# Kernel optimization log

Measured on AMD Instinct MI355X. Metric: run time of the kernel, lower is better.

The kernel has to match this reference:

```python
import jax, jax.numpy as jnp
import numpy as np

B, T, D = 2, 4096, 512
H, K = 8, 64
F = 2048
EPS = 1e-5


def _layer_norm(x, scale, offset):
    mean = jnp.mean(x, axis=-1, keepdims=True)
    var = jnp.var(x, axis=-1, keepdims=True)
    inv = scale * jax.lax.rsqrt(var + EPS)
    return (x - mean) * inv + offset


def setup_inputs() -> dict:
    key = jax.random.key(0)
    ks = jax.random.split(key, 12)
    s = lambda fan_in: (2.0 / fan_in) ** 0.5  # VarianceScaling(2.0) std
    inputs = jax.random.normal(ks[0], (B, T, D), jnp.float32)
    return {
        "inputs": inputs,
        "ln1_scale": jnp.ones((D,), jnp.float32),
        "ln1_offset": jnp.zeros((D,), jnp.float32),
        "wq": jax.random.normal(ks[1], (D, H * K), jnp.float32) * s(D),
        "bq": jnp.zeros((H * K,), jnp.float32),
        "wk": jax.random.normal(ks[2], (D, H * K), jnp.float32) * s(D),
        "bk": jnp.zeros((H * K,), jnp.float32),
        "wv": jax.random.normal(ks[3], (D, H * K), jnp.float32) * s(D),
        "bv": jnp.zeros((H * K,), jnp.float32),
        "wo": jax.random.normal(ks[4], (H * K, D), jnp.float32) * s(H * K),
        "bo": jnp.zeros((D,), jnp.float32),
        "ln2_scale": jnp.ones((D,), jnp.float32),
        "ln2_offset": jnp.zeros((D,), jnp.float32),
        "w1": jax.random.normal(ks[5], (D, F), jnp.float32) * (1.0 / D) ** 0.5,
        "b1": jnp.zeros((F,), jnp.float32),
        "w2": jax.random.normal(ks[6], (F, D), jnp.float32) * (1.0 / F) ** 0.5,
        "b2": jnp.zeros((D,), jnp.float32),
    }


def reference(inputs, ln1_scale, ln1_offset, wq, bq, wk, bk, wv, bv, wo, bo,
              ln2_scale, ln2_offset, w1, b1, w2, b2):
    # --- pre-attention LayerNorm ---
    x1 = _layer_norm(inputs, ln1_scale, ln1_offset)
    # --- multi-head attention (eval mode, no mask) ---
    q = (x1 @ wq + bq).reshape(B, T, H, K)
    k = (x1 @ wk + bk).reshape(B, T, H, K)
    v = (x1 @ wv + bv).reshape(B, T, H, K)
    logits = jnp.einsum('bthd,bshd->bhts', q, k) / jnp.sqrt(jnp.asarray(K, q.dtype))
    attn = jax.nn.softmax(logits, axis=-1)
    ctx = jnp.einsum('bhts,bshd->bthd', attn, v).reshape(B, T, H * K)
    attn_out = ctx @ wo + bo
    # --- residual ---
    x = inputs + attn_out
    # --- pre-FFN LayerNorm + GELU FFN ---
    y = _layer_norm(x, ln2_scale, ln2_offset)
    ff = jax.nn.gelu(y @ w1 + b1) @ w2 + b2
    return x + ff
```

## Files before the change

### kernel.cpp

```cpp
#include <hip/hip_runtime.h>
#include <hip/hip_bf16.h>

typedef __attribute__((ext_vector_type(4))) float f32x4;
typedef __attribute__((ext_vector_type(8))) short short8;

#define DEV __device__ __forceinline__

DEV short f2bf(float f) {
    union { float f; unsigned u; } a; a.f = f;
    unsigned r = a.u + 0x7fffu + ((a.u >> 16) & 1u);
    return (short)(r >> 16);
}

DEV float bf2f(short s) {
    union { unsigned u; float f; } a;
    a.u = ((unsigned)(unsigned short)s) << 16;
    return a.f;
}

DEV unsigned cvt_pk_bf16(float a, float b) {
    unsigned r;
    asm("v_cvt_pk_bf16_f32 %0, %1, %2" : "=v"(r) : "v"(a), "v"(b));
    return r;
}

DEV float exp2_fast(float x) { return __builtin_amdgcn_exp2f(x); }

DEV void gload16(const short* g, short* l) {
    __builtin_amdgcn_global_load_lds(
        (__attribute__((address_space(1))) void*)g,
        (__attribute__((address_space(3))) void*)l, 16, 0, 0);
}

DEV float gelu_f(float x) {
    float u = 0.7978845608028654f * (x + 0.044715f * x * x * x);
    float e = __expf(2.0f * u);
    float t = 1.0f - 2.0f / (e + 1.0f);
    return 0.5f * x * (1.0f + t);
}

__global__ __launch_bounds__(256) void ln_kernel(const float* __restrict__ x,
                                                 const float* __restrict__ scale,
                                                 const float* __restrict__ offset,
                                                 short* __restrict__ out) {
    const int wid = threadIdx.x >> 6, lane = threadIdx.x & 63;
    const long row = (long)blockIdx.x * 4 + wid;
    const float* xr = x + row * 512;
    f32x4 v0 = *(const f32x4*)&xr[lane * 8];
    f32x4 v1 = *(const f32x4*)&xr[lane * 8 + 4];
    float s = 0.f, sq = 0.f;
#pragma unroll
    for (int i = 0; i < 4; i++) {
        s += v0[i] + v1[i];
        sq += v0[i] * v0[i] + v1[i] * v1[i];
    }
#pragma unroll
    for (int m = 1; m < 64; m <<= 1) { s += __shfl_xor(s, m); sq += __shfl_xor(sq, m); }
    float mean = s * (1.0f / 512.0f);
    float var = sq * (1.0f / 512.0f) - mean * mean;
    float inv = rsqrtf(var + 1e-5f);
    f32x4 sc0 = *(const f32x4*)&scale[lane * 8];
    f32x4 sc1 = *(const f32x4*)&scale[lane * 8 + 4];
    f32x4 of0 = *(const f32x4*)&offset[lane * 8];
    f32x4 of1 = *(const f32x4*)&offset[lane * 8 + 4];
    short8 o;
#pragma unroll
    for (int i = 0; i < 4; i++) {
        o[i]     = f2bf((v0[i] - mean) * inv * sc0[i] + of0[i]);
        o[4 + i] = f2bf((v1[i] - mean) * inv * sc1[i] + of1[i]);
    }
    *(short8*)&out[row * 512 + lane * 8] = o;
}

__global__ __launch_bounds__(256) void prep_kernel(const float* __restrict__ wq,
                                                   const float* __restrict__ wk,
                                                   const float* __restrict__ wv,
                                                   const float* __restrict__ wo,
                                                   const float* __restrict__ w1,
                                                   const float* __restrict__ w2,
                                                   const float* __restrict__ bq,
                                                   const float* __restrict__ bk,
                                                   const float* __restrict__ bv,
                                                   short* __restrict__ wqkvt,
                                                   short* __restrict__ wot,
                                                   short* __restrict__ w1t,
                                                   short* __restrict__ w2t,
                                                   float* __restrict__ bqkv) {
    const int bid = blockIdx.x;
    if (bid == 768) {
        for (int i = threadIdx.x; i < 512; i += 256) {
            bqkv[i] = bq[i]; bqkv[512 + i] = bk[i]; bqkv[1024 + i] = bv[i];
        }
        return;
    }
    const float* src; short* dst; int Kd, N, kt, nt;
    if (bid < 256) {
        Kd = 512; N = 512;
        const int which = bid >> 6, local = bid & 63;
        kt = local & 7; nt = local >> 3;
        if (which == 0)      { src = wq; dst = wqkvt; }
        else if (which == 1) { src = wk; dst = wqkvt + 512 * 512; }
        else if (which == 2) { src = wv; dst = wqkvt + 2 * 512 * 512; }
        else                 { src = wo; dst = wot; }
    } else if (bid < 512) {
        src = w1; dst = w1t; Kd = 512; N = 2048;
        const int local = bid - 256; kt = local & 7; nt = local >> 3;
    } else {
        src = w2; dst = w2t; Kd = 2048; N = 512;
        const int local = bid - 512; kt = local & 31; nt = local >> 5;
    }
    __shared__ float tile[64][65];
    const int k0 = kt * 64, n0 = nt * 64;
    const int tid = threadIdx.x;
#pragma unroll
    for (int ld = 0; ld < 4; ld++) {
        int li = ld * 1024 + tid * 4;
        int r = li >> 6, c = li & 63;
        f32x4 tv = *(const f32x4*)&src[(long)(k0 + r) * N + n0 + c];
        tile[r][c] = tv[0]; tile[r][c + 1] = tv[1];
        tile[r][c + 2] = tv[2]; tile[r][c + 3] = tv[3];
    }
    __syncthreads();
#pragma unroll
    for (int st = 0; st < 2; st++) {
        int li = st * 2048 + tid * 8;
        int r = li >> 6, c = li & 63;
        short8 o;
#pragma unroll
        for (int i = 0; i < 8; i++) o[i] = f2bf(tile[c + i][r]);
        *(short8*)&dst[(long)(n0 + r) * Kd + k0 + c] = o;
    }
}

template <int BM, bool GELU_ACT, bool OUT_BF16, bool RESID>
__global__ __launch_bounds__(256) void gemm_bt(const short* __restrict__ A,
                                               const short* __restrict__ Bt,
                                               const float* __restrict__ bias,
                                               const float* __restrict__ resid,
                                               void* __restrict__ Cout,
                                               int M, int N, int Kd) {
    constexpr int NR = (BM == 128) ? 4 : 2;
    constexpr int LA = BM / 32;
    __shared__ short Asm[BM][64];
    __shared__ short Bsm[128][64];
    const int tid = threadIdx.x;
    const int wid = tid >> 6, lane = tid & 63;
    const int lr = lane & 15, lg = lane >> 4;
    const int row0 = blockIdx.x * BM, col0 = blockIdx.y * 128;
    const int wm = (BM == 128) ? (wid >> 1) * 64 : 0;
    const int wn = (BM == 128) ? (wid & 1) * 64 : wid * 32;

    f32x4 acc[4][NR];
#pragma unroll
    for (int m = 0; m < 4; m++)
#pragma unroll
        for (int n = 0; n < NR; n++)
#pragma unroll
            for (int j = 0; j < 4; j++) acc[m][n][j] = 0.f;

    const int swr = (lr & 7) << 3;

    for (int k0 = 0; k0 < Kd; k0 += 64) {
#pragma unroll
        for (int ld = 0; ld < LA; ld++) {
            int off = ld * 2048 + tid * 8;
            int r = off >> 6, c = off & 63;
            int sc = c ^ ((r & 7) << 3);
            gload16(&A[(long)(row0 + r) * Kd + k0 + sc], &Asm[0][0] + off);
        }
#pragma unroll
        for (int ld = 0; ld < 4; ld++) {
            int off = ld * 2048 + tid * 8;
            int r = off >> 6, c = off & 63;
            int sc = c ^ ((r & 7) << 3);
            gload16(&Bt[(long)(col0 + r) * Kd + k0 + sc], &Bsm[0][0] + off);
        }
        __syncthreads();
#pragma unroll
        for (int kk = 0; kk < 64; kk += 32) {
            short8 af[4], bf[NR];
#pragma unroll
            for (int m = 0; m < 4; m++) af[m] = *(const short8*)&Asm[wm + m * 16 + lr][(kk + lg * 8) ^ swr];
#pragma unroll
            for (int n = 0; n < NR; n++) bf[n] = *(const short8*)&Bsm[wn + n * 16 + lr][(kk + lg * 8) ^ swr];
#pragma unroll
            for (int m = 0; m < 4; m++)
#pragma unroll
                for (int n = 0; n < NR; n++)
                    acc[m][n] = __builtin_amdgcn_mfma_f32_16x16x32_bf16(af[m], bf[n], acc[m][n], 0, 0, 0);
        }
        __syncthreads();
    }

#pragma unroll
    for (int m = 0; m < 4; m++) {
#pragma unroll
        for (int n = 0; n < NR; n++) {
#pragma unroll
            for (int j = 0; j < 4; j++) {
                int r = row0 + wm + m * 16 + lg * 4 + j;
                int c = col0 + wn + n * 16 + lr;
                float v = acc[m][n][j] + bias[c];
                if constexpr (GELU_ACT) v = gelu_f(v);
                if constexpr (RESID) v += resid[(long)r * N + c];
                if constexpr (OUT_BF16) ((short*)Cout)[(long)r * N + c] = f2bf(v);
                else                    ((float*)Cout)[(long)r * N + c] = v;
            }
        }
    }
}

__global__ __launch_bounds__(256) void attn_kernel(const short* __restrict__ q,
                                                   const short* __restrict__ k,
                                                   const short* __restrict__ v,
                                                   float* __restrict__ opart,
                                                   float* __restrict__ mpart,
                                                   float* __restrict__ lpart) {
    __shared__ short Ksm[128][64];
    __shared__ short Vsm[64][136];
    __shared__ short Psm[4][16][136];
    const int tid = threadIdx.x, wid = tid >> 6, lane = tid & 63;
    const int lr = lane & 15, lg = lane >> 4;
    const int bh = blockIdx.y, b = bh >> 3, h = bh & 7;
    const int t0 = blockIdx.x * 128;
    const int split = blockIdx.z;
    const int s_begin = split * 2048, s_end = s_begin + 2048;
    const long base = (long)b * 4096 * 1536 + h * 64;

    short8 qf[2][2];
#pragma unroll
    for (int rg = 0; rg < 2; rg++) {
        const long qoff = base + (long)(t0 + wid * 32 + rg * 16 + lr) * 1536 + lg * 8;
        short8 q0 = *(const short8*)&q[qoff];
        short8 q1 = *(const short8*)&q[qoff + 32];
#pragma unroll
        for (int i = 0; i < 8; i++) {
            qf[rg][0][i] = f2bf(bf2f(q0[i]) * 0.18033688f);
            qf[rg][1][i] = f2bf(bf2f(q1[i]) * 0.18033688f);
        }
    }

    f32x4 o[2][4];
    float mrow[8], lrow[8];
#pragma unroll
    for (int rg = 0; rg < 2; rg++)
#pragma unroll
        for (int n = 0; n < 4; n++)
#pragma unroll
            for (int j = 0; j < 4; j++) o[rg][n][j] = 0.f;
#pragma unroll
    for (int j = 0; j < 8; j++) { mrow[j] = -1e30f; lrow[j] = 0.f; }

    const int skey = tid >> 3, sd = (tid & 7) * 8, sm = tid & 7;
    short8 kreg[4], vreg[4];
#pragma unroll
    for (int p = 0; p < 4; p++) {
        long off = base + (long)(s_begin + p * 32 + skey) * 1536 + sd;
        kreg[p] = *(const short8*)&k[off];
        vreg[p] = *(const short8*)&v[off];
    }

    for (int s0 = s_begin; s0 < s_end; s0 += 128) {
        __syncthreads();
#pragma unroll
        for (int p = 0; p < 4; p++) {
            int key = p * 32 + skey;
            *(short8*)&Ksm[key][sd ^ ((key & 7) << 3)] = kreg[p];
            int kc = key ^ (sm << 3);
#pragma unroll
            for (int i = 0; i < 8; i++) Vsm[sd + i][kc] = vreg[p][i];
        }
        __syncthreads();
        if (s0 + 128 < s_end) {
#pragma unroll
            for (int p = 0; p < 4; p++) {
                long off = base + (long)(s0 + 128 + p * 32 + skey) * 1536 + sd;
                kreg[p] = *(const short8*)&k[off];
                vreg[p] = *(const short8*)&v[off];
            }
        }

        const int ksw = (lr & 7) << 3;
#pragma unroll
        for (int rg = 0; rg < 2; rg++) {
            f32x4 s[8];
#pragma unroll
            for (int c = 0; c < 8; c++) { s[c][0] = 0.f; s[c][1] = 0.f; s[c][2] = 0.f; s[c][3] = 0.f; }
            __builtin_amdgcn_s_setprio(1);
#pragma unroll
            for (int c = 0; c < 8; c++) {
                const int krow = c * 16 + lr;
                short8 kf0 = *(const short8*)&Ksm[krow][(lg * 8) ^ ksw];
                short8 kf1 = *(const short8*)&Ksm[krow][(32 + lg * 8) ^ ksw];
                s[c] = __builtin_amdgcn_mfma_f32_16x16x32_bf16(qf[rg][0], kf0, s[c], 0, 0, 0);
                s[c] = __builtin_amdgcn_mfma_f32_16x16x32_bf16(qf[rg][1], kf1, s[c], 0, 0, 0);
            }
            __builtin_amdgcn_s_setprio(0);

#pragma unroll
            for (int j = 0; j < 4; j++) {
                const int r8 = rg * 4 + j;
                float m01 = fmaxf(s[0][j], s[1][j]), m23 = fmaxf(s[2][j], s[3][j]);
                float m45 = fmaxf(s[4][j], s[5][j]), m67 = fmaxf(s[6][j], s[7][j]);
                float mx = fmaxf(fmaxf(m01, m23), fmaxf(m45, m67));
                mx = fmaxf(mx, __shfl_xor(mx, 1));
                mx = fmaxf(mx, __shfl_xor(mx, 2));
                mx = fmaxf(mx, __shfl_xor(mx, 4));
                mx = fmaxf(mx, __shfl_xor(mx, 8));
                float mn = mrow[r8];
                if (!__all(mx <= mn + 8.0f)) {
                    mn = fmaxf(mrow[r8], mx);
                    float alpha = exp2_fast(mrow[r8] - mn);
                    mrow[r8] = mn;
                    lrow[r8] *= alpha;
#pragma unroll
                    for (int n = 0; n < 4; n++) o[rg][n][j] *= alpha;
                }
                float rs = 0.f;
#pragma unroll
                for (int c = 0; c < 8; c++) {
                    float e = exp2_fast(s[c][j] - mn);
                    s[c][j] = e;
                    rs += e;
                }
                rs += __shfl_xor(rs, 1);
                rs += __shfl_xor(rs, 2);
                rs += __shfl_xor(rs, 4);
                rs += __shfl_xor(rs, 8);
                lrow[r8] += rs;
            }

#pragma unroll
            for (int j = 0; j < 4; j++) {
                short* prow = &Psm[wid][lg * 4 + j][lr];
#pragma unroll
                for (int c = 0; c < 8; c += 2) {
                    unsigned pk = cvt_pk_bf16(s[c][j], s[c + 1][j]);
                    prow[c * 16]      = (short)(pk & 0xffff);
                    prow[c * 16 + 16] = (short)(pk >> 16);
                }
            }
            short8 pa[4];
#pragma unroll
            for (int kk = 0; kk < 4; kk++) pa[kk] = *(const short8*)&Psm[wid][lr][kk * 32 + lg * 8];

            __builtin_amdgcn_s_setprio(1);
#pragma unroll
            for (int n = 0; n < 4; n++) {
                const int vrow = n * 16 + lr;
                const int vsw = ((vrow >> 3) & 7) << 3;
#pragma unroll
                for (int kk = 0; kk < 4; kk++) {
                    short8 vf = *(const short8*)&Vsm[vrow][(kk * 32 + lg * 8) ^ vsw];
                    o[rg][n] = __builtin_amdgcn_mfma_f32_16x16x32_bf16(pa[kk], vf, o[rg][n], 0, 0, 0);
                }
            }
            __builtin_amdgcn_s_setprio(0);
        }
    }

    const long rowbase = (long)b * 4096 + t0 + wid * 32;
    const long ob = ((long)split * 8192 + rowbase) * 512 + h * 64;
#pragma unroll
    for (int rg = 0; rg < 2; rg++)
#pragma unroll
        for (int j = 0; j < 4; j++)
#pragma unroll
            for (int n = 0; n < 4; n++)
                opart[ob + (long)(rg * 16 + lg * 4 + j) * 512 + n * 16 + lr] = o[rg][n][j];
    if (lr == 0) {
#pragma unroll
        for (int rg = 0; rg < 2; rg++)
#pragma unroll
            for (int j = 0; j < 4; j++) {
                long idx = ((long)split * 8192 + rowbase + rg * 16 + lg * 4 + j) * 8 + h;
                mpart[idx] = mrow[rg * 4 + j];
                lpart[idx] = lrow[rg * 4 + j];
            }
    }
}

__global__ __launch_bounds__(256) void attn_merge(const float* __restrict__ op,
                                                  const float* __restrict__ mp,
                                                  const float* __restrict__ lp,
                                                  short* __restrict__ ctx) {
    const int wid = threadIdx.x >> 6, lane = threadIdx.x & 63;
    const long row = (long)blockIdx.x * 4 + wid;
    const int c0 = lane * 8, h = c0 >> 6;
    float m0 = mp[row * 8 + h], m1 = mp[(8192 + row) * 8 + h];
    float l0 = lp[row * 8 + h], l1 = lp[(8192 + row) * 8 + h];
    float M = fmaxf(m0, m1);
    float w0 = exp2_fast(m0 - M), w1 = exp2_fast(m1 - M);
    float inv = 1.0f / (w0 * l0 + w1 * l1);
    w0 *= inv; w1 *= inv;
    f32x4 a0 = *(const f32x4*)&op[row * 512 + c0];
    f32x4 a1 = *(const f32x4*)&op[row * 512 + c0 + 4];
    f32x4 b0 = *(const f32x4*)&op[(8192 + row) * 512 + c0];
    f32x4 b1 = *(const f32x4*)&op[(8192 + row) * 512 + c0 + 4];
    short8 o;
#pragma unroll
    for (int i = 0; i < 4; i++) {
        o[i]     = f2bf(w0 * a0[i] + w1 * b0[i]);
        o[4 + i] = f2bf(w0 * a1[i] + w1 * b1[i]);
    }
    *(short8*)&ctx[row * 512 + c0] = o;
}

extern "C" void kernel_launch(void* const* d_in, const int* in_sizes, int n_in,
                              void* d_out, int out_size, void* d_ws, size_t ws_size,
                              hipStream_t stream) {
    (void)in_sizes; (void)n_in; (void)out_size; (void)ws_size;
    const float* inputs = (const float*)d_in[0];
    const float* ln1_s  = (const float*)d_in[1];
    const float* ln1_o  = (const float*)d_in[2];
    const float* wq     = (const float*)d_in[3];
    const float* bq     = (const float*)d_in[4];
    const float* wk     = (const float*)d_in[5];
    const float* bk     = (const float*)d_in[6];
    const float* wv     = (const float*)d_in[7];
    const float* bv     = (const float*)d_in[8];
    const float* wo     = (const float*)d_in[9];
    const float* bo     = (const float*)d_in[10];
    const float* ln2_s  = (const float*)d_in[11];
    const float* ln2_o  = (const float*)d_in[12];
    const float* w1     = (const float*)d_in[13];
    const float* b1     = (const float*)d_in[14];
    const float* w2     = (const float*)d_in[15];
    const float* b2     = (const float*)d_in[16];
    float* out = (float*)d_out;

    char* p = (char*)d_ws;
    auto alloc = [&](size_t bytes) { void* r = (void*)p; p += (bytes + 255) & ~(size_t)255; return r; };
    short* x1    = (short*)alloc((size_t)8192 * 512 * 2);
    short* qkvb  = (short*)alloc((size_t)8192 * 1536 * 2);
    short* ctxb  = (short*)alloc((size_t)8192 * 512 * 2);
    short* yb    = (short*)alloc((size_t)8192 * 512 * 2);
    short* hb    = (short*)alloc((size_t)8192 * 2048 * 2);
    short* wqkvt = (short*)alloc((size_t)1536 * 512 * 2);
    short* wot   = (short*)alloc((size_t)512 * 512 * 2);
    short* w1t   = (short*)alloc((size_t)2048 * 512 * 2);
    short* w2t   = (short*)alloc((size_t)512 * 2048 * 2);
    float* bqkv  = (float*)alloc((size_t)1536 * 4);
    float* opart = (float*)alloc((size_t)2 * 8192 * 512 * 4);
    float* mpart = (float*)alloc((size_t)2 * 8192 * 8 * 4);
    float* lpart = (float*)alloc((size_t)2 * 8192 * 8 * 4);

    dim3 blk(256);
    prep_kernel<<<769, blk, 0, stream>>>(wq, wk, wv, wo, w1, w2, bq, bk, bv,
                                         wqkvt, wot, w1t, w2t, bqkv);
    ln_kernel<<<2048, blk, 0, stream>>>(inputs, ln1_s, ln1_o, x1);
    gemm_bt<128, false, true, false><<<dim3(64, 12), blk, 0, stream>>>(x1, wqkvt, bqkv, nullptr, qkvb, 8192, 1536, 512);
    attn_kernel<<<dim3(32, 16, 2), blk, 0, stream>>>(qkvb, qkvb + 512, qkvb + 1024, opart, mpart, lpart);
    attn_merge<<<2048, blk, 0, stream>>>(opart, mpart, lpart, ctxb);
    gemm_bt<64, false, false, true><<<dim3(128, 4), blk, 0, stream>>>(ctxb, wot, bo, inputs, out, 8192, 512, 512);
    ln_kernel<<<2048, blk, 0, stream>>>(out, ln2_s, ln2_o, yb);
    gemm_bt<128, true, true, false><<<dim3(64, 16), blk, 0, stream>>>(yb, w1t, b1, nullptr, hb, 8192, 2048, 512);
    gemm_bt<64, false, false, true><<<dim3(128, 4), blk, 0, stream>>>(hb, w2t, b2, out, out, 8192, 512, 2048);
}
```

Measured before the change: 407.4 us.

## Transpose QK^T MFMA so each lane owns one query row in softmax

Swaps the MFMA operand order so the score tile comes out transposed, which puts each query row on a single lane column. The row max and sum then need fewer cross-lane shuffles (two instead of four per row group) and fewer per-row state registers. P is written to shared memory with packed 8-byte stores instead of scalar 2-byte stores. Rescaling the output accumulators now needs a per-row shuffle of alpha, and the stored m/l values are written by the first 16 lanes.

```diff
diff --git a/kernel.cpp b/kernel.cpp
--- a/kernel.cpp
+++ b/kernel.cpp
@@ -3,6 +3,7 @@
 
 typedef __attribute__((ext_vector_type(4))) float f32x4;
 typedef __attribute__((ext_vector_type(8))) short short8;
+typedef __attribute__((ext_vector_type(2))) unsigned u32x2;
 
 #define DEV __device__ __forceinline__
 
@@ -241,15 +242,15 @@
     }
 
     f32x4 o[2][4];
-    float mrow[8], lrow[8];
-#pragma unroll
-    for (int rg = 0; rg < 2; rg++)
+    float mrow[2], lrow[2];
+#pragma unroll
+    for (int rg = 0; rg < 2; rg++) {
+        mrow[rg] = -1e30f; lrow[rg] = 0.f;
 #pragma unroll
         for (int n = 0; n < 4; n++)
 #pragma unroll
             for (int j = 0; j < 4; j++) o[rg][n][j] = 0.f;
-#pragma unroll
-    for (int j = 0; j < 8; j++) { mrow[j] = -1e30f; lrow[j] = 0.f; }
+    }
 
     const int skey = tid >> 3, sd = (tid & 7) * 8, sm = tid & 7;
     short8 kreg[4], vreg[4];
@@ -292,53 +293,52 @@
                 const int krow = c * 16 + lr;
                 short8 kf0 = *(const short8*)&Ksm[krow][(lg * 8) ^ ksw];
                 short8 kf1 = *(const short8*)&Ksm[krow][(32 + lg * 8) ^ ksw];
-                s[c] = __builtin_amdgcn_mfma_f32_16x16x32_bf16(qf[rg][0], kf0, s[c], 0, 0, 0);
-                s[c] = __builtin_amdgcn_mfma_f32_16x16x32_bf16(qf[rg][1], kf1, s[c], 0, 0, 0);
+                s[c] = __builtin_amdgcn_mfma_f32_16x16x32_bf16(kf0, qf[rg][0], s[c], 0, 0, 0);
+                s[c] = __builtin_amdgcn_mfma_f32_16x16x32_bf16(kf1, qf[rg][1], s[c], 0, 0, 0);
             }
             __builtin_amdgcn_s_setprio(0);
 
-#pragma unroll
-            for (int j = 0; j < 4; j++) {
-                const int r8 = rg * 4 + j;
-                float m01 = fmaxf(s[0][j], s[1][j]), m23 = fmaxf(s[2][j], s[3][j]);
-                float m45 = fmaxf(s[4][j], s[5][j]), m67 = fmaxf(s[6][j], s[7][j]);
-                float mx = fmaxf(fmaxf(m01, m23), fmaxf(m45, m67));
-                mx = fmaxf(mx, __shfl_xor(mx, 1));
-                mx = fmaxf(mx, __shfl_xor(mx, 2));
-                mx = fmaxf(mx, __shfl_xor(mx, 4));
-                mx = fmaxf(mx, __shfl_xor(mx, 8));
-                float mn = mrow[r8];
-                if (!__all(mx <= mn + 8.0f)) {
-                    mn = fmaxf(mrow[r8], mx);
-                    float alpha = exp2_fast(mrow[r8] - mn);
-                    mrow[r8] = mn;
-                    lrow[r8] *= alpha;
-#pragma unroll
-                    for (int n = 0; n < 4; n++) o[rg][n][j] *= alpha;
+            f32x4 m4 = s[0];
+#pragma unroll
+            for (int c = 1; c < 8; c++)
+#pragma unroll
+                for (int j = 0; j < 4; j++) m4[j] = fmaxf(m4[j], s[c][j]);
+            float mx = fmaxf(fmaxf(m4[0], m4[1]), fmaxf(m4[2], m4[3]));
+            mx = fmaxf(mx, __shfl_xor(mx, 16));
+            mx = fmaxf(mx, __shfl_xor(mx, 32));
+            float mn = mrow[rg];
+            if (!__all(mx <= mn + 8.0f)) {
+                mn = fmaxf(mrow[rg], mx);
+                float alpha = exp2_fast(mrow[rg] - mn);
+                mrow[rg] = mn;
+                lrow[rg] *= alpha;
+#pragma unroll
+                for (int j = 0; j < 4; j++) {
+                    float aj = __shfl(alpha, lg * 4 + j);
+#pragma unroll
+                    for (int n = 0; n < 4; n++) o[rg][n][j] *= aj;
                 }
-                float rs = 0.f;
-#pragma unroll
-                for (int c = 0; c < 8; c++) {
+            }
+            f32x4 sum4 = {0.f, 0.f, 0.f, 0.f};
+#pragma unroll
+            for (int c = 0; c < 8; c++)
+#pragma unroll
+                for (int j = 0; j < 4; j++) {
                     float e = exp2_fast(s[c][j] - mn);
                     s[c][j] = e;
-                    rs += e;
+                    sum4[j] += e;
                 }
-                rs += __shfl_xor(rs, 1);
-                rs += __shfl_xor(rs, 2);
-                rs += __shfl_xor(rs, 4);
-                rs += __shfl_xor(rs, 8);
-                lrow[r8] += rs;
-            }
-
-#pragma unroll
-            for (int j = 0; j < 4; j++) {
-                short* prow = &Psm[wid][lg * 4 + j][lr];
-#pragma unroll
-                for (int c = 0; c < 8; c += 2) {
-                    unsigned pk = cvt_pk_bf16(s[c][j], s[c + 1][j]);
-                    prow[c * 16]      = (short)(pk & 0xffff);
-                    prow[c * 16 + 16] = (short)(pk >> 16);
-                }
+            float rs = (sum4[0] + sum4[1]) + (sum4[2] + sum4[3]);
+            rs += __shfl_xor(rs, 16);
+            rs += __shfl_xor(rs, 32);
+            lrow[rg] += rs;
+
+#pragma unroll
+            for (int c = 0; c < 8; c++) {
+                u32x2 w;
+                w[0] = cvt_pk_bf16(s[c][0], s[c][1]);
+                w[1] = cvt_pk_bf16(s[c][2], s[c][3]);
+                *(u32x2*)&Psm[wid][lr][c * 16 + lg * 4] = w;
             }
             short8 pa[4];
 #pragma unroll
@@ -368,15 +368,13 @@
 #pragma unroll
             for (int n = 0; n < 4; n++)
                 opart[ob + (long)(rg * 16 + lg * 4 + j) * 512 + n * 16 + lr] = o[rg][n][j];
-    if (lr == 0) {
-#pragma unroll
-        for (int rg = 0; rg < 2; rg++)
-#pragma unroll
-            for (int j = 0; j < 4; j++) {
-                long idx = ((long)split * 8192 + rowbase + rg * 16 + lg * 4 + j) * 8 + h;
-                mpart[idx] = mrow[rg * 4 + j];
-                lpart[idx] = lrow[rg * 4 + j];
-            }
+    if (lane < 16) {
+#pragma unroll
+        for (int rg = 0; rg < 2; rg++) {
+            long idx = ((long)split * 8192 + rowbase + rg * 16 + lr) * 8 + h;
+            mpart[idx] = mrow[rg];
+            lpart[idx] = lrow[rg];
+        }
     }
 }
 
```

Result: faster. 350.5 us (-14.0%).
